# Performance work log

Measured on AMD Instinct MI355X. Metric: run time of the kernel, lower is better.

## Reference

```python
import jax, jax.numpy as jnp
import numpy as np

HEAD_SIZE = 64


def setup_inputs() -> dict:
    key = jax.random.key(0)
    ks = jax.random.split(key, 6)
    B, S, D, H = 8, 2048, 1024, HEAD_SIZE
    return {
        "q": jax.random.normal(ks[0], (B, S, D), dtype=jnp.float32),
        "k": jax.random.normal(ks[1], (B, S, D), dtype=jnp.float32),
        "v": jax.random.normal(ks[2], (B, S, D), dtype=jnp.float32),
        "mask": jnp.ones((B, S), dtype=bool),
        "Wq": jax.random.normal(ks[3], (D, H), dtype=jnp.float32) * (D ** -0.5),
        "Wk": jax.random.normal(ks[4], (D, H), dtype=jnp.float32) * (D ** -0.5),
        "Wv": jax.random.normal(ks[5], (D, H), dtype=jnp.float32) * (D ** -0.5),
    }


def reference(q, k, v, mask, Wq, Wk, Wv):
    # Linear projections (bias=False): x @ W, W is [n_embd, head_size]
    qp = jnp.einsum("bsd,dh->bsh", q, Wq)
    kp = jnp.einsum("bsd,dh->bsh", k, Wk)
    vp = jnp.einsum("bsd,dh->bsh", v, Wv)
    scale = HEAD_SIZE ** -0.5
    scores = jnp.einsum("bqh,bkh->bqk", qp, kp) * scale  # [B, Sq, Sk]
    # 2-D mask [B, Sk] -> broadcast over query dim (mask.unsqueeze(1))
    scores = jnp.where(mask[:, None, :], scores, -jnp.inf)
    attn = jax.nn.softmax(scores, axis=-1)
    # dropout is identity in eval mode (deterministic reference)
    out = jnp.einsum("bqk,bkh->bqh", attn, vp)
    return out
```

## Files before the change

kernel.cpp:

```cpp
#include <hip/hip_runtime.h>
#include <hip/hip_bf16.h>
#include <math.h>

#define B_ 8
#define S_ 2048
#define D_ 1024
#define H_ 64
#define M_ (B_*S_)
#define SPLIT 4
#define KPS (S_/SPLIT)

typedef __attribute__((ext_vector_type(8))) short bf16x8;
typedef __attribute__((ext_vector_type(8))) unsigned short u16x8;
typedef __attribute__((ext_vector_type(4))) float f32x4;

__device__ inline unsigned short f2bf(float f) {
    unsigned int u = __builtin_bit_cast(unsigned int, f);
    u += 0x7fffu + ((u >> 16) & 1u);
    return (unsigned short)(u >> 16);
}

__device__ inline void async16(const void* g, void* l) {
    __builtin_amdgcn_global_load_lds((const __attribute__((address_space(1))) void*)g,
                                     (__attribute__((address_space(3))) void*)l, 16, 0, 0);
}

__global__ __launch_bounds__(256) void mask_kernel(const unsigned char* __restrict__ mask,
                                                   float* __restrict__ mmul, int n) {
    int j = blockIdx.x * 256 + threadIdx.x;
    if (j >= n) return;
    bool boolLayout = mask[1] != 0;
    int mv = boolLayout ? (int)mask[j] : ((const int*)mask)[j];
    mmul[j] = mv ? 1.0f : 0.0f;
}

__global__ __launch_bounds__(256) void wprep_kernel(
    const float* __restrict__ Wq, const float* __restrict__ Wk, const float* __restrict__ Wv,
    unsigned short* __restrict__ Wt)
{
    const int m = blockIdx.y;
    const float* W = (m == 0) ? Wq : (m == 1) ? Wk : Wv;
    unsigned short* Wo = Wt + (size_t)m * 64 * 1024;
    __shared__ unsigned short T[64][65];
    const int t = threadIdx.x;
    const int k0 = blockIdx.x * 64;
    #pragma unroll
    for (int i = 0; i < 16; i++) {
        int vi = t + i * 256;
        int kk = vi >> 6, n = vi & 63;
        T[kk][n] = f2bf(W[(size_t)(k0 + kk) * 64 + n]);
    }
    __syncthreads();
    #pragma unroll
    for (int i = 0; i < 4; i++) {
        int vi = t + i * 256;
        int n = vi >> 4, k4 = vi & 15;
        ushort4 u;
        u.x = T[k4*4+0][n]; u.y = T[k4*4+1][n]; u.z = T[k4*4+2][n]; u.w = T[k4*4+3][n];
        *(ushort4*)&Wo[(size_t)n * 1024 + k0 + k4*4] = u;
    }
}

__global__ __launch_bounds__(256) void proj_kernel(
    const float* __restrict__ q, const float* __restrict__ kx, const float* __restrict__ vx,
    const unsigned short* __restrict__ Wt,
    unsigned short* __restrict__ qp, unsigned short* __restrict__ kp, unsigned short* __restrict__ vpT)
{
    __shared__ float          Ax[64 * 128];
    __shared__ unsigned short Wl[64 * 128];

    const int m = blockIdx.y;
    const float* x = (m == 0) ? q : (m == 1) ? kx : vx;
    const unsigned short* Wm = Wt + (size_t)m * 64 * 1024;

    const int t = threadIdx.x;
    const int w = t >> 6, l = t & 63;
    const int lrow = l & 15, quad = l >> 4;
    const int row0 = blockIdx.x * 64;

    f32x4 acc[4] = {};

    for (int ks = 0; ks < D_; ks += 128) {
        __syncthreads();
        #pragma unroll
        for (int j = 0; j < 8; j++) {
            int p = (w * 8 + j) * 64 + l;
            int r = p >> 5;
            int cc = (p & 31) ^ (r & 7);
            async16(&x[(size_t)(row0 + r) * D_ + ks + cc * 4], &Ax[p * 4]);
        }
        #pragma unroll
        for (int j = 0; j < 4; j++) {
            int p = (w * 4 + j) * 64 + l;
            int n = p >> 4;
            int kc = (p & 15) ^ (n & 7);
            async16(&Wm[(size_t)n * 1024 + ks + kc * 8], &Wl[p * 8]);
        }
        __syncthreads();

        const int r = w * 16 + lrow;
        #pragma unroll
        for (int kk = 0; kk < 4; kk++) {
            const int c32 = kk * 8 + quad * 2;
            f32x4 a0 = *(const f32x4*)&Ax[(r * 32 + ((c32    ) ^ (r & 7))) * 4];
            f32x4 a1 = *(const f32x4*)&Ax[(r * 32 + ((c32 + 1) ^ (r & 7))) * 4];
            bf16x8 af;
            af[0] = (short)f2bf(a0.x); af[1] = (short)f2bf(a0.y);
            af[2] = (short)f2bf(a0.z); af[3] = (short)f2bf(a0.w);
            af[4] = (short)f2bf(a1.x); af[5] = (short)f2bf(a1.y);
            af[6] = (short)f2bf(a1.z); af[7] = (short)f2bf(a1.w);
            #pragma unroll
            for (int c = 0; c < 4; c++) {
                const int n = c * 16 + lrow;
                bf16x8 bf = *(const bf16x8*)&Wl[(n * 16 + ((kk * 4 + quad) ^ (n & 7))) * 8];
                acc[c] = __builtin_amdgcn_mfma_f32_16x16x32_bf16(af, bf, acc[c], 0, 0, 0);
            }
        }
    }

    const int orow = row0 + w * 16 + quad * 4;
    if (m < 2) {
        unsigned short* outp = (m == 0) ? qp : kp;
        const float sc = (m == 0) ? 0.125f : 1.0f;
        #pragma unroll
        for (int c = 0; c < 4; c++)
            #pragma unroll
            for (int rr = 0; rr < 4; rr++)
                outp[(size_t)(orow + rr) * H_ + c * 16 + lrow] = f2bf(acc[c][rr]);
        if (m == 0) {
            #pragma unroll
            for (int c = 0; c < 4; c++)
                #pragma unroll
                for (int rr = 0; rr < 4; rr++)
                    outp[(size_t)(orow + rr) * H_ + c * 16 + lrow] = f2bf(acc[c][rr] * sc);
        }
    } else {
        const int bb = orow >> 11;
        const int s0 = orow & (S_ - 1);
        #pragma unroll
        for (int c = 0; c < 4; c++) {
            ushort4 u;
            u.x = f2bf(acc[c][0]); u.y = f2bf(acc[c][1]);
            u.z = f2bf(acc[c][2]); u.w = f2bf(acc[c][3]);
            *(ushort4*)&vpT[((size_t)bb * H_ + c * 16 + lrow) * S_ + s0] = u;
        }
    }
}

__global__ __launch_bounds__(256) void attn_kernel(
    const unsigned short* __restrict__ qp, const unsigned short* __restrict__ kp,
    const unsigned short* __restrict__ vpT, const float* __restrict__ mmul,
    float* __restrict__ po, float* __restrict__ pl)
{
    __shared__ unsigned short Qs[64][72];
    __shared__ unsigned short Ps[64][72];
    __shared__ unsigned short Ks[64 * 64];
    __shared__ unsigned short Vt[64 * 64];

    const int t = threadIdx.x;
    const int w = t >> 6, l = t & 63;
    const int lrow = l & 15, quad = l >> 4;
    const int b = blockIdx.y, q0 = blockIdx.x * 64, split = blockIdx.z;
    const int key0 = split * KPS;
    const size_t basebs = (size_t)b * S_;
    const unsigned short* vb = vpT + (size_t)b * H_ * S_;

    #pragma unroll
    for (int i = 0; i < 2; i++) {
        int p = t + i * 256;
        int r = p >> 3, c8 = p & 7;
        u16x8 u = *(const u16x8*)&qp[(basebs + q0 + r) * H_ + c8 * 8];
        *(u16x8*)&Qs[r][c8 * 8] = u;
    }

    float lsum[4] = {0.f, 0.f, 0.f, 0.f};
    f32x4 o[4] = {};

    for (int kt = 0; kt < KPS / 64; kt++) {
        const int k0 = key0 + kt * 64;
        __syncthreads();
        #pragma unroll
        for (int j = 0; j < 2; j++) {
            int p = (w * 2 + j) * 64 + l;
            int r = p >> 3;
            int c8 = (p & 7) ^ (r & 7);
            async16(&kp[(basebs + k0 + r) * H_ + c8 * 8], &Ks[p * 8]);
        }
        #pragma unroll
        for (int j = 0; j < 2; j++) {
            int p = (w * 2 + j) * 64 + l;
            int h = p >> 3;
            int c8 = (p & 7) ^ (h & 7);
            async16(&vb[(size_t)h * S_ + k0 + c8 * 8], &Vt[p * 8]);
        }
        float mm[4];
        #pragma unroll
        for (int c = 0; c < 4; c++) mm[c] = mmul[basebs + k0 + c*16 + lrow];
        __syncthreads();

        f32x4 s[4] = {};
        #pragma unroll
        for (int kk = 0; kk < 2; kk++) {
            bf16x8 aq = *(const bf16x8*)&Qs[w*16 + lrow][kk*32 + quad*8];
            #pragma unroll
            for (int c = 0; c < 4; c++) {
                const int n = c*16 + lrow;
                bf16x8 bk = *(const bf16x8*)&Ks[(n * 8 + ((kk*4 + quad) ^ (n & 7))) * 8];
                s[c] = __builtin_amdgcn_mfma_f32_16x16x32_bf16(aq, bk, s[c], 0, 0, 0);
            }
        }
        #pragma unroll
        for (int r = 0; r < 4; r++) {
            float p0 = __expf(s[0][r]) * mm[0];
            float p1 = __expf(s[1][r]) * mm[1];
            float p2 = __expf(s[2][r]) * mm[2];
            float p3 = __expf(s[3][r]) * mm[3];
            lsum[r] += (p0 + p1) + (p2 + p3);
            const int pr = w*16 + quad*4 + r;
            Ps[pr][ 0 + lrow] = f2bf(p0);
            Ps[pr][16 + lrow] = f2bf(p1);
            Ps[pr][32 + lrow] = f2bf(p2);
            Ps[pr][48 + lrow] = f2bf(p3);
        }
        #pragma unroll
        for (int kk = 0; kk < 2; kk++) {
            bf16x8 ap = *(const bf16x8*)&Ps[w*16 + lrow][kk*32 + quad*8];
            #pragma unroll
            for (int c = 0; c < 4; c++) {
                const int h = c*16 + lrow;
                bf16x8 bv = *(const bf16x8*)&Vt[(h * 8 + ((kk*4 + quad) ^ (h & 7))) * 8];
                o[c] = __builtin_amdgcn_mfma_f32_16x16x32_bf16(ap, bv, o[c], 0, 0, 0);
            }
        }
    }

    float* pob = po + (size_t)split * M_ * H_;
    float* plb = pl + (size_t)split * M_;
    #pragma unroll
    for (int r = 0; r < 4; r++) {
        #pragma unroll
        for (int d = 1; d < 16; d <<= 1)
            lsum[r] += __shfl_xor(lsum[r], d, 64);
        const size_t row = basebs + q0 + w*16 + quad*4 + r;
        if (lrow == 0) plb[row] = lsum[r];
        #pragma unroll
        for (int c = 0; c < 4; c++)
            pob[row * H_ + c*16 + lrow] = o[c][r];
    }
}

__global__ __launch_bounds__(256) void combine_kernel(
    const float* __restrict__ po, const float* __restrict__ pl, float* __restrict__ out)
{
    const int idx = blockIdx.x * 256 + threadIdx.x;
    const size_t row = idx >> 4;
    const int c4 = (idx & 15) * 4;
    float lt = 0.f;
    #pragma unroll
    for (int s = 0; s < SPLIT; s++) lt += pl[(size_t)s * M_ + row];
    f32x4 acc = {};
    #pragma unroll
    for (int s = 0; s < SPLIT; s++) {
        const f32x4 p = *(const f32x4*)&po[((size_t)s * M_ + row) * H_ + c4];
        acc += p;
    }
    const float inv = 1.0f / lt;
    f32x4 r = acc * inv;
    *(f32x4*)&out[row * H_ + c4] = r;
}

extern "C" void kernel_launch(void* const* d_in, const int* in_sizes, int n_in,
                              void* d_out, int out_size, void* d_ws, size_t ws_size,
                              hipStream_t stream) {
    const float* q  = (const float*)d_in[0];
    const float* k  = (const float*)d_in[1];
    const float* v  = (const float*)d_in[2];
    const unsigned char* mask = (const unsigned char*)d_in[3];
    const float* Wq = (const float*)d_in[4];
    const float* Wk = (const float*)d_in[5];
    const float* Wv = (const float*)d_in[6];
    float* out = (float*)d_out;

    unsigned short* qp  = (unsigned short*)d_ws;
    unsigned short* kp  = qp + (size_t)M_ * H_;
    unsigned short* vpT = kp + (size_t)M_ * H_;
    float* mmul = (float*)(vpT + (size_t)M_ * H_);
    unsigned short* Wt = (unsigned short*)(mmul + M_);
    float* po = (float*)(Wt + (size_t)3 * 64 * 1024);
    float* pl = po + (size_t)SPLIT * M_ * H_;

    wprep_kernel<<<dim3(16, 3), dim3(256), 0, stream>>>(Wq, Wk, Wv, Wt);
    mask_kernel<<<dim3((M_ + 255)/256), dim3(256), 0, stream>>>(mask, mmul, M_);
    proj_kernel<<<dim3(M_/64, 3), dim3(256), 0, stream>>>(q, k, v, Wt, qp, kp, vpT);
    attn_kernel<<<dim3(S_/64, B_, SPLIT), dim3(256), 0, stream>>>(qp, kp, vpT, mmul, po, pl);
    combine_kernel<<<dim3(M_*16/256), dim3(256), 0, stream>>>(po, pl, out);
}
```

Baseline: 244.3 us.

## Double-buffer projection K-chunks with async LDS loads overlapping MFMA compute

The projection kernel now stages the input and weight tiles in 64-wide K chunks across two LDS buffers. It issues the next chunk's async global-to-LDS loads before computing on the current one, with manual vmcnt waits and barriers. This hides global load latency behind the MFMA work. It also removes the duplicated store for the Q output, which had been written twice, the second time scaled. The costs are more barriers per K step and a fragile hand-written waitcnt count.

```diff
diff --git a/kernel.cpp b/kernel.cpp
--- a/kernel.cpp
+++ b/kernel.cpp
@@ -66,8 +66,8 @@
     const unsigned short* __restrict__ Wt,
     unsigned short* __restrict__ qp, unsigned short* __restrict__ kp, unsigned short* __restrict__ vpT)
 {
-    __shared__ float          Ax[64 * 128];
-    __shared__ unsigned short Wl[64 * 128];
+    __shared__ float          Ax[2][64 * 64];
+    __shared__ unsigned short Wl[2][64 * 64];
 
     const int m = blockIdx.y;
     const float* x = (m == 0) ? q : (m == 1) ? kx : vx;
@@ -80,30 +80,30 @@
 
     f32x4 acc[4] = {};
 
-    for (int ks = 0; ks < D_; ks += 128) {
-        __syncthreads();
-        #pragma unroll
-        for (int j = 0; j < 8; j++) {
-            int p = (w * 8 + j) * 64 + l;
-            int r = p >> 5;
-            int cc = (p & 31) ^ (r & 7);
-            async16(&x[(size_t)(row0 + r) * D_ + ks + cc * 4], &Ax[p * 4]);
-        }
+    auto issue = [&](int ks, int bi) {
         #pragma unroll
         for (int j = 0; j < 4; j++) {
-            int p = (w * 4 + j) * 64 + l;
-            int n = p >> 4;
-            int kc = (p & 15) ^ (n & 7);
-            async16(&Wm[(size_t)n * 1024 + ks + kc * 8], &Wl[p * 8]);
-        }
-        __syncthreads();
-
+            int p = j * 256 + t;
+            int r = p >> 4;
+            int cc = (p & 15) ^ (r & 7);
+            async16(&x[(size_t)(row0 + r) * D_ + ks + cc * 4], &Ax[bi][p * 4]);
+        }
+        #pragma unroll
+        for (int j = 0; j < 2; j++) {
+            int p = j * 256 + t;
+            int n = p >> 3;
+            int kc = (p & 7) ^ (n & 7);
+            async16(&Wm[(size_t)n * 1024 + ks + kc * 8], &Wl[bi][p * 8]);
+        }
+    };
+
+    auto compute = [&](int bi) {
         const int r = w * 16 + lrow;
         #pragma unroll
-        for (int kk = 0; kk < 4; kk++) {
-            const int c32 = kk * 8 + quad * 2;
-            f32x4 a0 = *(const f32x4*)&Ax[(r * 32 + ((c32    ) ^ (r & 7))) * 4];
-            f32x4 a1 = *(const f32x4*)&Ax[(r * 32 + ((c32 + 1) ^ (r & 7))) * 4];
+        for (int kk = 0; kk < 2; kk++) {
+            const int c0 = kk * 8 + quad * 2;
+            f32x4 a0 = *(const f32x4*)&Ax[bi][(r * 16 + ((c0    ) ^ (r & 7))) * 4];
+            f32x4 a1 = *(const f32x4*)&Ax[bi][(r * 16 + ((c0 + 1) ^ (r & 7))) * 4];
             bf16x8 af;
             af[0] = (short)f2bf(a0.x); af[1] = (short)f2bf(a0.y);
             af[2] = (short)f2bf(a0.z); af[3] = (short)f2bf(a0.w);
@@ -112,11 +112,22 @@
             #pragma unroll
             for (int c = 0; c < 4; c++) {
                 const int n = c * 16 + lrow;
-                bf16x8 bf = *(const bf16x8*)&Wl[(n * 16 + ((kk * 4 + quad) ^ (n & 7))) * 8];
+                bf16x8 bf = *(const bf16x8*)&Wl[bi][(n * 8 + ((kk * 4 + quad) ^ (n & 7))) * 8];
                 acc[c] = __builtin_amdgcn_mfma_f32_16x16x32_bf16(af, bf, acc[c], 0, 0, 0);
             }
         }
-    }
+    };
+
+    issue(0, 0);
+    #pragma unroll 1
+    for (int kc = 0; kc < 15; kc++) {
+        issue((kc + 1) * 64, (kc + 1) & 1);
+        asm volatile("s_waitcnt vmcnt(6)\n\ts_barrier" ::: "memory");
+        compute(kc & 1);
+        asm volatile("s_barrier" ::: "memory");
+    }
+    asm volatile("s_waitcnt vmcnt(0)\n\ts_barrier" ::: "memory");
+    compute(1);
 
     const int orow = row0 + w * 16 + quad * 4;
     if (m < 2) {
@@ -126,14 +137,7 @@
         for (int c = 0; c < 4; c++)
             #pragma unroll
             for (int rr = 0; rr < 4; rr++)
-                outp[(size_t)(orow + rr) * H_ + c * 16 + lrow] = f2bf(acc[c][rr]);
-        if (m == 0) {
-            #pragma unroll
-            for (int c = 0; c < 4; c++)
-                #pragma unroll
-                for (int rr = 0; rr < 4; rr++)
-                    outp[(size_t)(orow + rr) * H_ + c * 16 + lrow] = f2bf(acc[c][rr] * sc);
-        }
+                outp[(size_t)(orow + rr) * H_ + c * 16 + lrow] = f2bf(acc[c][rr] * sc);
     } else {
         const int bb = orow >> 11;
         const int s0 = orow & (S_ - 1);
```

Result: no change. 243.2 us (-0.4%).
